# Optimization experiments

Hardware: AMD Instinct MI355X
Metric: run time of the kernel (lower is better)

The kernel has to match this reference:

```python
import jax, jax.numpy as jnp
import numpy as np

B, T = 32, 8192
RNN, ENC, ATT, LOC, K = 1024, 512, 128, 32, 31


def setup_inputs() -> dict:
    key = jax.random.key(0)
    ks = jax.random.split(key, 9)
    return {
        'queries': jax.random.normal(ks[0], (B, RNN), jnp.float32),
        'memories': jax.random.normal(ks[1], (B, ENC, T), jnp.float32),
        'processed_memories': jax.random.normal(ks[2], (B, ATT, T), jnp.float32),
        'previous_alignments': jax.random.uniform(ks[3], (B, T), jnp.float32),
        'cumulated_alignments': jax.random.uniform(ks[4], (B, T), jnp.float32),
        'masks': jnp.zeros((B, T), jnp.bool_),
        # learned params (xavier-ish scale)
        'w_query': jax.random.normal(ks[5], (ATT, RNN), jnp.float32) * (1.0 / np.sqrt(RNN)),
        'w_loc_conv': jax.random.normal(ks[6], (LOC, 2, K), jnp.float32) * (1.0 / np.sqrt(2 * K)),
        'w_loc_1x1': jax.random.normal(ks[7], (ATT, LOC), jnp.float32) * (1.0 / np.sqrt(LOC)),
        'w_score': jax.random.normal(ks[8], (ATT,), jnp.float32) * (1.0 / np.sqrt(ATT)),
    }


def reference(queries, memories, processed_memories, previous_alignments,
              cumulated_alignments, masks, w_query, w_loc_conv, w_loc_1x1, w_score):
    # ---- Calc_Score ----
    # Query 1x1 conv == matmul: [B, ATT, 1]
    q = (queries @ w_query.T)[:, :, None]
    # Location features: conv over [B, 2, T] (same padding), then 1x1 -> [B, ATT, T]
    attn_cat = jnp.stack([previous_alignments, cumulated_alignments], axis=1)  # [B,2,T]
    pad = (K - 1) // 2
    loc = jax.lax.conv_general_dilated(attn_cat, w_loc_conv, (1,), [(pad, pad)],
                                       dimension_numbers=('NCH', 'OIH', 'NCH'))  # [B,LOC,T]
    loc = jnp.einsum('blt,al->bat', loc, w_loc_1x1)  # [B,ATT,T]
    scores = jnp.einsum('bat,a->bt', jnp.tanh(q + processed_memories + loc), w_score)  # [B,T]
    # ---- Apply_Score (sigmoid_noise = 0) ----
    scores = jnp.where(masks, -jnp.finfo(scores.dtype).max, scores)
    p = jax.nn.sigmoid(scores)  # p_choose_i, [B,T]
    # stepwise monotonic update: a_t = prev*p + shift_right(prev*(1-p))
    shifted = jnp.pad((previous_alignments * (1.0 - p))[:, :-1], ((0, 0), (1, 0)))
    alignments = previous_alignments * p + shifted  # [B,T]
    contexts = jnp.einsum('bt,bct->bc', alignments, memories)  # [B,ENC]
    return contexts, alignments
```

## Files before the change

kernel.cpp:

```cpp
#include <hip/hip_runtime.h>
#include <math.h>

#define B_   32
#define T_   8192
#define RNN_ 1024
#define ENC_ 512
#define ATT_ 128
#define LOC_ 32
#define K_   31
#define PAD_ 15

__device__ __forceinline__ float fast_tanh(float x) {
    x = fminf(15.f, fmaxf(-15.f, x));
    float e = __expf(2.f * x);
    return (e - 1.f) * __builtin_amdgcn_rcpf(e + 1.f);
}

__device__ __forceinline__ float fast_sigmoid(float x) {
    x = fminf(30.f, fmaxf(-30.f, x));
    float e = __expf(-x);
    return __builtin_amdgcn_rcpf(1.f + e);
}

__global__ __launch_bounds__(256) void k_query(const float* __restrict__ queries,
                                               const float* __restrict__ wq,
                                               float* __restrict__ qout) {
    int w    = blockIdx.x * 4 + (threadIdx.x >> 6);
    int lane = threadIdx.x & 63;
    int b = w >> 7, a = w & 127;
    const float4* qrow = (const float4*)(queries + (size_t)b * RNN_);
    const float4* wrow = (const float4*)(wq + (size_t)a * RNN_);
    float acc = 0.f;
#pragma unroll
    for (int i = 0; i < 4; ++i) {
        float4 x = qrow[i * 64 + lane];
        float4 y = wrow[i * 64 + lane];
        acc += x.x * y.x + x.y * y.y + x.z * y.z + x.w * y.w;
    }
#pragma unroll
    for (int off = 32; off; off >>= 1) acc += __shfl_xor(acc, off);
    if (lane == 0) qout[b * ATT_ + a] = acc;
}

__global__ void k_prep(const float* __restrict__ w, float* __restrict__ wT) {
    for (int i = threadIdx.x; i < LOC_ * 2 * K_; i += blockDim.x) {
        int l = i / (2 * K_);
        int rem = i % (2 * K_);
        int c = rem / K_;
        int k = rem % K_;
        wT[k * (2 * LOC_) + c * LOC_ + l] = w[i];
    }
}

#define VT    2
#define BLK2  256
#define TILE2 (BLK2 * VT)

__global__ __launch_bounds__(256) void k_score(
    const float* __restrict__ pm,
    const float* __restrict__ prev,
    const float* __restrict__ cum,
    const unsigned char* __restrict__ masks,
    const float* __restrict__ qbuf,
    const float* __restrict__ wT,
    const float* __restrict__ w1,
    const float* __restrict__ wsc,
    float* __restrict__ pout)
{
    __shared__ float sP[TILE2 + K_ - 1];
    __shared__ float sC[TILE2 + K_ - 1];
    int blk  = blockIdx.x;
    int b    = blk >> 4;
    int tile = blk & 15;
    int tbase = tile * TILE2;
    const float* prow = prev + (size_t)b * T_;
    const float* crow = cum + (size_t)b * T_;
    for (int i = threadIdx.x; i < TILE2 + K_ - 1; i += BLK2) {
        int g = tbase - PAD_ + i;
        bool ok = (g >= 0) && (g < T_);
        sP[i] = ok ? prow[g] : 0.f;
        sC[i] = ok ? crow[g] : 0.f;
    }
    __syncthreads();

    int lt = threadIdx.x * VT;
    int t0 = tbase + lt;

    float loc[LOC_][VT];
#pragma unroll
    for (int l = 0; l < LOC_; ++l)
#pragma unroll
        for (int j = 0; j < VT; ++j) loc[l][j] = 0.f;

    for (int k = 0; k < K_; ++k) {
        float pv[VT], cv[VT];
#pragma unroll
        for (int j = 0; j < VT; ++j) {
            pv[j] = sP[lt + k + j];
            cv[j] = sC[lt + k + j];
        }
        const float* wk = wT + k * (2 * LOC_);
#pragma unroll
        for (int l = 0; l < LOC_; ++l) {
            float wp = wk[l];
            float wc = wk[LOC_ + l];
#pragma unroll
            for (int j = 0; j < VT; ++j)
                loc[l][j] = fmaf(wp, pv[j], fmaf(wc, cv[j], loc[l][j]));
        }
    }

    float score0 = 0.f, score1 = 0.f;
    const float* pmb = pm + (size_t)b * ATT_ * T_ + t0;
    const float* qb  = qbuf + b * ATT_;
    for (int a = 0; a < ATT_; ++a) {
        float q   = qb[a];
        float wsa = wsc[a];
        const float* w1a = w1 + a * LOC_;
        float2 pmv = *(const float2*)(pmb + (size_t)a * T_);
        float l20 = 0.f, l21 = 0.f;
#pragma unroll
        for (int l = 0; l < LOC_; ++l) {
            float wv = w1a[l];
            l20 = fmaf(wv, loc[l][0], l20);
            l21 = fmaf(wv, loc[l][1], l21);
        }
        score0 += wsa * fast_tanh(q + pmv.x + l20);
        score1 += wsa * fast_tanh(q + pmv.y + l21);
    }

    unsigned char m0 = masks[(size_t)b * T_ + t0];
    unsigned char m1 = masks[(size_t)b * T_ + t0 + 1];
    float s0 = m0 ? -3.0e38f : score0;
    float s1 = m1 ? -3.0e38f : score1;
    float2 out;
    out.x = fast_sigmoid(s0);
    out.y = fast_sigmoid(s1);
    *(float2*)(pout + (size_t)b * T_ + t0) = out;
}

__global__ __launch_bounds__(256) void k_align(const float* __restrict__ p,
                                               const float* __restrict__ prev,
                                               float* __restrict__ align) {
    int idx = blockIdx.x * blockDim.x + threadIdx.x;
    int b  = idx / (T_ / 4);
    int t0 = (idx % (T_ / 4)) * 4;
    const float* pr = p + (size_t)b * T_;
    const float* vr = prev + (size_t)b * T_;
    float4 p4 = *(const float4*)(pr + t0);
    float4 v4 = *(const float4*)(vr + t0);
    float pm1 = (t0 > 0) ? pr[t0 - 1] : 0.f;
    float vm1 = (t0 > 0) ? vr[t0 - 1] : 0.f;
    float4 o;
    o.x = v4.x * p4.x + vm1 * (1.f - pm1);
    o.y = v4.y * p4.y + v4.x * (1.f - p4.x);
    o.z = v4.z * p4.z + v4.y * (1.f - p4.y);
    o.w = v4.w * p4.w + v4.z * (1.f - p4.z);
    *(float4*)(align + (size_t)b * T_ + t0) = o;
}

__global__ __launch_bounds__(256) void k_context(const float* __restrict__ mem,
                                                 const float* __restrict__ align,
                                                 float* __restrict__ ctx) {
    int w    = blockIdx.x * 4 + (threadIdx.x >> 6);
    int lane = threadIdx.x & 63;
    int b = w >> 9;
    int c = w & 511;
    const float4* mrow = (const float4*)(mem + ((size_t)b * ENC_ + c) * T_);
    const float4* arow = (const float4*)(align + (size_t)b * T_);
    float acc = 0.f;
#pragma unroll 4
    for (int i = 0; i < T_ / 256; ++i) {
        float4 m = mrow[i * 64 + lane];
        float4 a = arow[i * 64 + lane];
        acc += m.x * a.x + m.y * a.y + m.z * a.z + m.w * a.w;
    }
#pragma unroll
    for (int off = 32; off; off >>= 1) acc += __shfl_xor(acc, off);
    if (lane == 0) ctx[b * ENC_ + c] = acc;
}

extern "C" void kernel_launch(void* const* d_in, const int* in_sizes, int n_in,
                              void* d_out, int out_size, void* d_ws, size_t ws_size,
                              hipStream_t stream) {
    const float* queries = (const float*)d_in[0];
    const float* memories = (const float*)d_in[1];
    const float* pm = (const float*)d_in[2];
    const float* prev = (const float*)d_in[3];
    const float* cum = (const float*)d_in[4];
    const unsigned char* masks = (const unsigned char*)d_in[5];
    const float* w_query = (const float*)d_in[6];
    const float* w_conv = (const float*)d_in[7];
    const float* w_1x1 = (const float*)d_in[8];
    const float* w_score = (const float*)d_in[9];

    float* out_ctx = (float*)d_out;
    float* out_align = (float*)d_out + (size_t)B_ * ENC_;

    float* ws_q = (float*)d_ws;
    float* ws_p = ws_q + B_ * ATT_;
    float* ws_wT = ws_p + (size_t)B_ * T_;

    hipLaunchKernelGGL(k_prep, dim3(1), dim3(256), 0, stream, w_conv, ws_wT);
    hipLaunchKernelGGL(k_query, dim3((B_ * ATT_) / 4), dim3(256), 0, stream,
                       queries, w_query, ws_q);
    hipLaunchKernelGGL(k_score, dim3(B_ * (T_ / TILE2)), dim3(BLK2), 0, stream,
                       pm, prev, cum, masks, ws_q, ws_wT, w_1x1, w_score, ws_p);
    hipLaunchKernelGGL(k_align, dim3((B_ * T_ / 4) / 256), dim3(256), 0, stream,
                       ws_p, prev, out_align);
    hipLaunchKernelGGL(k_context, dim3((B_ * ENC_) / 4), dim3(256), 0, stream,
                       memories, out_align, out_ctx);
}
```

Baseline: 192.0 us.

## Fuse alignment update into split-T context reduction and merge prep with query kernel

Merges the conv-weight transpose into the query kernel as an extra block, saving one launch. The alignment update is fused with the context dot product: each block computes a 512-wide alignment tile into shared memory, then reduces all 512 encoder channels over that tile into per-tile partial sums. A small reduction kernel adds the 16 partials per (b,c). This removes the round trip that re-read alignments from global memory and changes the context parallelism from one wave per channel over all T to T-tiles, at the cost of a partial buffer and an extra launch.

```diff
diff --git a/kernel.cpp b/kernel.cpp
--- a/kernel.cpp
+++ b/kernel.cpp
@@ -22,9 +22,21 @@
     return __builtin_amdgcn_rcpf(1.f + e);
 }
 
-__global__ __launch_bounds__(256) void k_query(const float* __restrict__ queries,
-                                               const float* __restrict__ wq,
-                                               float* __restrict__ qout) {
+__global__ __launch_bounds__(256) void k_prep_query(const float* __restrict__ queries,
+                                                    const float* __restrict__ wq,
+                                                    const float* __restrict__ wconv,
+                                                    float* __restrict__ qout,
+                                                    float* __restrict__ wT) {
+    if (blockIdx.x == (B_ * ATT_) / 4) {
+        for (int i = threadIdx.x; i < LOC_ * 2 * K_; i += blockDim.x) {
+            int l = i / (2 * K_);
+            int rem = i % (2 * K_);
+            int c = rem / K_;
+            int k = rem % K_;
+            wT[k * (2 * LOC_) + c * LOC_ + l] = wconv[i];
+        }
+        return;
+    }
     int w    = blockIdx.x * 4 + (threadIdx.x >> 6);
     int lane = threadIdx.x & 63;
     int b = w >> 7, a = w & 127;
@@ -40,16 +52,6 @@
 #pragma unroll
     for (int off = 32; off; off >>= 1) acc += __shfl_xor(acc, off);
     if (lane == 0) qout[b * ATT_ + a] = acc;
-}
-
-__global__ void k_prep(const float* __restrict__ w, float* __restrict__ wT) {
-    for (int i = threadIdx.x; i < LOC_ * 2 * K_; i += blockDim.x) {
-        int l = i / (2 * K_);
-        int rem = i % (2 * K_);
-        int c = rem / K_;
-        int k = rem % K_;
-        wT[k * (2 * LOC_) + c * LOC_ + l] = w[i];
-    }
 }
 
 #define VT    2
@@ -139,45 +141,68 @@
     *(float2*)(pout + (size_t)b * T_ + t0) = out;
 }
 
-__global__ __launch_bounds__(256) void k_align(const float* __restrict__ p,
-                                               const float* __restrict__ prev,
-                                               float* __restrict__ align) {
-    int idx = blockIdx.x * blockDim.x + threadIdx.x;
-    int b  = idx / (T_ / 4);
-    int t0 = (idx % (T_ / 4)) * 4;
+#define TILE3 512
+__global__ __launch_bounds__(256) void k_align_ctx(
+    const float* __restrict__ p,
+    const float* __restrict__ prev,
+    const float* __restrict__ mem,
+    float* __restrict__ align_out,
+    float* __restrict__ part)
+{
+    __shared__ float sA[TILE3];
+    int blk  = blockIdx.x;
+    int b    = blk >> 4;
+    int tile = blk & 15;
+    int tbase = tile * TILE3;
     const float* pr = p + (size_t)b * T_;
     const float* vr = prev + (size_t)b * T_;
-    float4 p4 = *(const float4*)(pr + t0);
-    float4 v4 = *(const float4*)(vr + t0);
+
+    int lt = threadIdx.x * 2;
+    int t0 = tbase + lt;
+    float2 p2 = *(const float2*)(pr + t0);
+    float2 v2 = *(const float2*)(vr + t0);
     float pm1 = (t0 > 0) ? pr[t0 - 1] : 0.f;
     float vm1 = (t0 > 0) ? vr[t0 - 1] : 0.f;
-    float4 o;
-    o.x = v4.x * p4.x + vm1 * (1.f - pm1);
-    o.y = v4.y * p4.y + v4.x * (1.f - p4.x);
-    o.z = v4.z * p4.z + v4.y * (1.f - p4.y);
-    o.w = v4.w * p4.w + v4.z * (1.f - p4.z);
-    *(float4*)(align + (size_t)b * T_ + t0) = o;
-}
-
-__global__ __launch_bounds__(256) void k_context(const float* __restrict__ mem,
-                                                 const float* __restrict__ align,
-                                                 float* __restrict__ ctx) {
-    int w    = blockIdx.x * 4 + (threadIdx.x >> 6);
+    float a0 = v2.x * p2.x + vm1 * (1.f - pm1);
+    float a1 = v2.y * p2.y + v2.x * (1.f - p2.x);
+    sA[lt] = a0;
+    sA[lt + 1] = a1;
+    float2 ao; ao.x = a0; ao.y = a1;
+    *(float2*)(align_out + (size_t)b * T_ + t0) = ao;
+    __syncthreads();
+
+    int wv   = threadIdx.x >> 6;
     int lane = threadIdx.x & 63;
-    int b = w >> 9;
-    int c = w & 511;
-    const float4* mrow = (const float4*)(mem + ((size_t)b * ENC_ + c) * T_);
-    const float4* arow = (const float4*)(align + (size_t)b * T_);
-    float acc = 0.f;
+    float av[8];
+#pragma unroll
+    for (int j = 0; j < 4; ++j) {
+        av[j]     = sA[4 * lane + j];
+        av[4 + j] = sA[256 + 4 * lane + j];
+    }
+    const float* mb = mem + ((size_t)b * ENC_) * T_ + tbase;
+
 #pragma unroll 4
-    for (int i = 0; i < T_ / 256; ++i) {
-        float4 m = mrow[i * 64 + lane];
-        float4 a = arow[i * 64 + lane];
-        acc += m.x * a.x + m.y * a.y + m.z * a.z + m.w * a.w;
-    }
-#pragma unroll
-    for (int off = 32; off; off >>= 1) acc += __shfl_xor(acc, off);
-    if (lane == 0) ctx[b * ENC_ + c] = acc;
+    for (int cc = 0; cc < 128; ++cc) {
+        int c = wv * 128 + cc;
+        const float4* mrow = (const float4*)(mb + (size_t)c * T_);
+        float4 m0 = mrow[lane];
+        float4 m1 = mrow[64 + lane];
+        float acc = m0.x * av[0] + m0.y * av[1] + m0.z * av[2] + m0.w * av[3]
+                  + m1.x * av[4] + m1.y * av[5] + m1.z * av[6] + m1.w * av[7];
+#pragma unroll
+        for (int off = 32; off; off >>= 1) acc += __shfl_xor(acc, off);
+        if (lane == 0) part[((size_t)b * ENC_ + c) * 16 + tile] = acc;
+    }
+}
+
+__global__ __launch_bounds__(256) void k_reduce(const float* __restrict__ part,
+                                                float* __restrict__ ctx) {
+    int idx = blockIdx.x * blockDim.x + threadIdx.x;
+    const float4* pr = (const float4*)(part + (size_t)idx * 16);
+    float4 a = pr[0], b = pr[1], c = pr[2], d = pr[3];
+    float s = a.x + a.y + a.z + a.w + b.x + b.y + b.z + b.w
+            + c.x + c.y + c.z + c.w + d.x + d.y + d.z + d.w;
+    ctx[idx] = s;
 }
 
 extern "C" void kernel_launch(void* const* d_in, const int* in_sizes, int n_in,
@@ -200,14 +225,14 @@
     float* ws_q = (float*)d_ws;
     float* ws_p = ws_q + B_ * ATT_;
     float* ws_wT = ws_p + (size_t)B_ * T_;
-
-    hipLaunchKernelGGL(k_prep, dim3(1), dim3(256), 0, stream, w_conv, ws_wT);
-    hipLaunchKernelGGL(k_query, dim3((B_ * ATT_) / 4), dim3(256), 0, stream,
-                       queries, w_query, ws_q);
+    float* ws_part = ws_wT + 1984;
+
+    hipLaunchKernelGGL(k_prep_query, dim3((B_ * ATT_) / 4 + 1), dim3(256), 0, stream,
+                       queries, w_query, w_conv, ws_q, ws_wT);
     hipLaunchKernelGGL(k_score, dim3(B_ * (T_ / TILE2)), dim3(BLK2), 0, stream,
                        pm, prev, cum, masks, ws_q, ws_wT, w_1x1, w_score, ws_p);
-    hipLaunchKernelGGL(k_align, dim3((B_ * T_ / 4) / 256), dim3(256), 0, stream,
-                       ws_p, prev, out_align);
-    hipLaunchKernelGGL(k_context, dim3((B_ * ENC_) / 4), dim3(256), 0, stream,
-                       memories, out_align, out_ctx);
-}
+    hipLaunchKernelGGL(k_align_ctx, dim3(B_ * (T_ / TILE3)), dim3(256), 0, stream,
+                       ws_p, prev, memories, out_align, ws_part);
+    hipLaunchKernelGGL(k_reduce, dim3((B_ * ENC_) / 256), dim3(256), 0, stream,
+                       ws_part, out_ctx);
+}
```

Measured after the change: 222.4 us. +15.8%, slower.
